# Optimization experiments

Measured on AMD Instinct MI355X. Metric: run time of the kernel, lower is better.

Reference implementation:

```python
import jax, jax.numpy as jnp
import numpy as np

N_NODES = 100000
DEG = 32
N_EDGES = N_NODES * DEG
N_FEAT = 128
N_CLASSES = 40
LN_EPS = 1e-5
CLAMP_MIN = 1e-5


def setup_inputs() -> dict:
    key = jax.random.key(0)
    k_h, k_lg, k_z, k_src, k_t1, k_t2 = jax.random.split(key, 6)
    h = jax.random.normal(k_h, (N_NODES, N_FEAT), dtype=jnp.float32)
    logits = jax.random.normal(k_lg, (N_NODES, N_CLASSES), dtype=jnp.float32)
    old_z = jax.random.uniform(k_z, (N_NODES,), dtype=jnp.float32)
    # uniform in-degree graph: every node receives exactly DEG messages
    dst = jnp.repeat(jnp.arange(N_NODES, dtype=jnp.int32), DEG)
    src = jax.random.randint(k_src, (N_EDGES,), 0, N_NODES, dtype=jnp.int32)
    in_degs = jnp.full((N_NODES,), float(DEG), dtype=jnp.float32)
    norm = 1.0 / in_degs  # GCN-style normalization constant per node
    tau_1 = jax.random.uniform(k_t1, (1,), dtype=jnp.float32)
    tau_2 = jax.random.uniform(k_t2, (1,), dtype=jnp.float32)
    return {"h": h, "logits": logits, "old_z": old_z, "norm": norm,
            "in_degs": in_degs, "tau_1": tau_1, "tau_2": tau_2,
            "src": src, "dst": dst}


def _node_layernorm(x):
    # LayerNorm over the node dimension, no affine (elementwise_affine=False)
    m = jnp.mean(x)
    v = jnp.var(x)
    return (x - m) * jax.lax.rsqrt(v + LN_EPS)


def reference(h, logits, old_z, norm, in_degs, tau_1, tau_2, src, dst):
    n = h.shape[0]
    c = logits.shape[1]
    # per-node predicted class, and per-edge neighbor prediction
    pred = jnp.argmax(logits, axis=1)            # [N]
    nbr_pred = pred[src]                          # [E]
    # f1: fraction of in-neighbors agreeing with the center node's prediction
    match = (nbr_pred == pred[dst]).astype(h.dtype)
    f1 = jax.ops.segment_sum(match, dst, num_segments=n) / in_degs
    # f2: entropy of the neighbor-prediction histogram per node
    counts = jnp.zeros((n, c), dtype=h.dtype).at[dst, nbr_pred].add(1.0)
    cnts_p = jnp.clip(counts / in_degs[:, None], CLAMP_MIN)
    f2 = -jnp.sum(cnts_p * jnp.log(cnts_p), axis=1)
    # both metrics are detached in the original
    f1 = jax.lax.stop_gradient(f1)
    f2 = jax.lax.stop_gradient(f2)
    norm_f1 = _node_layernorm(f1)
    norm_f2 = _node_layernorm(f2)
    # shared_tau=True path: uses externally provided tau_1 / tau_2
    z = jax.nn.sigmoid(-(norm_f1 - tau_1)) * jax.nn.sigmoid(-(norm_f2 - tau_2))
    gate = jnp.minimum(old_z, z)
    # sum aggregation of neighbor features, normalized and activated
    agg = jax.ops.segment_sum(h[src], dst, num_segments=n)   # [N, F]
    normagg = jax.nn.relu(agg * norm[:, None])
    new_h = h + gate[:, None] * normagg
    return new_h, z
```

## Files before the change

### kernel.cpp

```cpp
#include <hip/hip_runtime.h>
#include <math.h>

#define N_NODES 100000
#define DEG 32
#define N_FEAT 128
#define N_CLASSES 40

constexpr float LN_EPS = 1e-5f;
constexpr float E0 = 1.1512925465e-4f;

#define NODE_ITERS 8
#define NODES_PER_BLOCK 64
#define NB2 ((N_NODES + NODES_PER_BLOCK - 1) / NODES_PER_BLOCK)

#define NCHUNK 4
#define AGG_NPB 192
#define NBLK ((N_NODES + AGG_NPB - 1) / AGG_NPB)

typedef float    f4 __attribute__((ext_vector_type(4)));
typedef float    f2 __attribute__((ext_vector_type(2)));
typedef int      i4 __attribute__((ext_vector_type(4)));
typedef unsigned u2 __attribute__((ext_vector_type(2)));
typedef unsigned u4 __attribute__((ext_vector_type(4)));

__device__ __forceinline__ unsigned pk4_fp8(float a, float b, float c, float d) {
    int w = __builtin_amdgcn_cvt_pk_fp8_f32(a, b, 0, false);
    w = __builtin_amdgcn_cvt_pk_fp8_f32(c, d, w, true);
    return (unsigned)w;
}
__device__ __forceinline__ void accp8(float* a, u2 r) {
    f2 p;
    p = __builtin_amdgcn_cvt_pk_f32_fp8((int)r.x, false); a[0] += p.x; a[1] += p.y;
    p = __builtin_amdgcn_cvt_pk_f32_fp8((int)r.x, true);  a[2] += p.x; a[3] += p.y;
    p = __builtin_amdgcn_cvt_pk_f32_fp8((int)r.y, false); a[4] += p.x; a[5] += p.y;
    p = __builtin_amdgcn_cvt_pk_f32_fp8((int)r.y, true);  a[6] += p.x; a[7] += p.y;
}

__global__ void k_prep(const float* __restrict__ logits, const float* __restrict__ h,
                       const float* __restrict__ old_z, const float* __restrict__ normv,
                       unsigned char* __restrict__ predb, f2* __restrict__ ozn,
                       unsigned char* __restrict__ hb8, int do_pack) {
    int t = blockIdx.x * 256 + threadIdx.x;
    if (t >= N_NODES * 4) return;
    int node = t >> 2;
    int q    = t & 3;

    const f2* lp = (const f2*)(logits + (size_t)node * N_CLASSES + q * 10);
    float best = -INFINITY;
    int bidx = 0;
#pragma unroll
    for (int i = 0; i < 5; ++i) {
        f2 v = lp[i];
        int i0 = q * 10 + 2 * i;
        if (v.x > best) { best = v.x; bidx = i0; }
        if (v.y > best) { best = v.y; bidx = i0 + 1; }
    }
#pragma unroll
    for (int off = 1; off < 4; off <<= 1) {
        float ov = __shfl_xor(best, off, 4);
        int   oi = __shfl_xor(bidx, off, 4);
        if (ov > best || (ov == best && oi < bidx)) { best = ov; bidx = oi; }
    }
    if (q == 0) {
        predb[node] = (unsigned char)bidx;
        f2 oz; oz.x = old_z[node]; oz.y = normv[node];
        ozn[node] = oz;
    }

    if (do_pack) {
        const f4* hp = (const f4*)(h + (size_t)node * N_FEAT + q * 32);
        f4 v0 = __builtin_nontemporal_load(hp + 0);
        f4 v1 = __builtin_nontemporal_load(hp + 1);
        f4 v2 = __builtin_nontemporal_load(hp + 2);
        f4 v3 = __builtin_nontemporal_load(hp + 3);
        f4 v4 = __builtin_nontemporal_load(hp + 4);
        f4 v5 = __builtin_nontemporal_load(hp + 5);
        f4 v6 = __builtin_nontemporal_load(hp + 6);
        f4 v7 = __builtin_nontemporal_load(hp + 7);
        u4 o0, o1;
        o0.x = pk4_fp8(v0.x, v0.y, v0.z, v0.w);
        o0.y = pk4_fp8(v1.x, v1.y, v1.z, v1.w);
        o0.z = pk4_fp8(v2.x, v2.y, v2.z, v2.w);
        o0.w = pk4_fp8(v3.x, v3.y, v3.z, v3.w);
        o1.x = pk4_fp8(v4.x, v4.y, v4.z, v4.w);
        o1.y = pk4_fp8(v5.x, v5.y, v5.z, v5.w);
        o1.z = pk4_fp8(v6.x, v6.y, v6.z, v6.w);
        o1.w = pk4_fp8(v7.x, v7.y, v7.z, v7.w);
        u4* op = (u4*)(hb8 + ((size_t)q * N_NODES + node) * 32);
        op[0] = o0;
        op[1] = o1;
    }
}

__global__ void k_f1f2(const int* __restrict__ src,
                       const unsigned char* __restrict__ predb,
                       f2* __restrict__ f12, float* __restrict__ part) {
    const int tid  = threadIdx.x;
    const int lane = tid & 63;
    const int wave = tid >> 6;
    const int grp  = lane >> 5;
    const int j    = lane & 31;

    float acc_s1 = 0.f, acc_q1 = 0.f, acc_s2 = 0.f, acc_q2 = 0.f;

    for (int t = 0; t < NODE_ITERS; ++t) {
        int node = blockIdx.x * NODES_PER_BLOCK + t * 8 + wave * 2 + grp;
        if (node < N_NODES) {
            int s = src[node * DEG + j];
            int v = predb[s];
            int pv = predb[node];
            int c = 0;
#pragma unroll
            for (int k = 0; k < 32; ++k)
                c += (v == __shfl(v, k, 32)) ? 1 : 0;
            float cf = (float)c;
            float p  = cf * (1.0f / 32.0f);
            float ent  = (-p * logf(p)) / cf;
            float dstc = 1.0f / cf;
            float mt   = (v == pv) ? 1.0f : 0.0f;
#pragma unroll
            for (int off = 16; off >= 1; off >>= 1) {
                mt   += __shfl_xor(mt, off, 32);
                ent  += __shfl_xor(ent, off, 32);
                dstc += __shfl_xor(dstc, off, 32);
            }
            if (j == 0) {
                float f1v = mt * (1.0f / 32.0f);
                float f2v = ent + ((float)N_CLASSES - dstc) * E0;
                f2 o; o.x = f1v; o.y = f2v;
                f12[node] = o;
                acc_s1 += f1v; acc_q1 += f1v * f1v;
                acc_s2 += f2v; acc_q2 += f2v * f2v;
            }
        }
    }

#pragma unroll
    for (int off = 1; off < 64; off <<= 1) {
        acc_s1 += __shfl_xor(acc_s1, off);
        acc_q1 += __shfl_xor(acc_q1, off);
        acc_s2 += __shfl_xor(acc_s2, off);
        acc_q2 += __shfl_xor(acc_q2, off);
    }
    __shared__ float4 sred[4];
    if (lane == 0) sred[wave] = make_float4(acc_s1, acc_q1, acc_s2, acc_q2);
    __syncthreads();
    if (tid == 0) {
        float4 r = sred[0];
        for (int w = 1; w < 4; ++w) {
            float4 q = sred[w];
            r.x += q.x; r.y += q.y; r.z += q.z; r.w += q.w;
        }
        part[0 * NB2 + blockIdx.x] = r.x;
        part[1 * NB2 + blockIdx.x] = r.y;
        part[2 * NB2 + blockIdx.x] = r.z;
        part[3 * NB2 + blockIdx.x] = r.w;
    }
}

__global__ void k_scal(const float* __restrict__ part, float* __restrict__ scal,
                       int* __restrict__ ctr) {
    const int tid = threadIdx.x;
    if (tid < 16) ctr[tid] = 0;
    double s1 = 0, q1 = 0, s2 = 0, q2 = 0;
    for (int i = tid; i < NB2; i += 256) {
        s1 += (double)part[0 * NB2 + i];
        q1 += (double)part[1 * NB2 + i];
        s2 += (double)part[2 * NB2 + i];
        q2 += (double)part[3 * NB2 + i];
    }
    __shared__ double sd[256][4];
    sd[tid][0] = s1; sd[tid][1] = q1; sd[tid][2] = s2; sd[tid][3] = q2;
    __syncthreads();
    for (int st = 128; st > 0; st >>= 1) {
        if (tid < st) {
            sd[tid][0] += sd[tid + st][0];
            sd[tid][1] += sd[tid + st][1];
            sd[tid][2] += sd[tid + st][2];
            sd[tid][3] += sd[tid + st][3];
        }
        __syncthreads();
    }
    if (tid == 0) {
        double n = (double)N_NODES;
        double m1 = sd[0][0] / n, v1 = sd[0][1] / n - m1 * m1;
        double m2 = sd[0][2] / n, v2 = sd[0][3] / n - m2 * m2;
        scal[0] = (float)m1;
        scal[1] = (float)(1.0 / sqrt(v1 + (double)LN_EPS));
        scal[2] = (float)m2;
        scal[3] = (float)(1.0 / sqrt(v2 + (double)LN_EPS));
    }
}

__global__ __launch_bounds__(256, 2) void k_aggc(
        const unsigned char* __restrict__ hb8, const float* __restrict__ h,
        const int* __restrict__ src, const f2* __restrict__ f12,
        const f2* __restrict__ ozn, const float* __restrict__ scal,
        const float* __restrict__ tau1, const float* __restrict__ tau2,
        int* __restrict__ ctr, float* __restrict__ out_h,
        float* __restrict__ out_z) {
    __shared__ int s_item;
    if (threadIdx.x == 0) {
        unsigned xcd;
        asm volatile("s_getreg_b32 %0, hwreg(HW_REG_XCC_ID)" : "=s"(xcd));
        xcd &= 3;
        int item = -1;
        for (int a = 0; a < NCHUNK; ++a) {
            int cc = (int)((xcd + a) & 3);
            int t = atomicAdd(&ctr[cc], 1);
            if (t < NBLK) { item = (cc << 16) | t; break; }
        }
        s_item = item;
    }
    __syncthreads();
    int item = s_item;
    if (item < 0) return;
    const int chunk = item >> 16;
    const int nb    = item & 0xffff;
    const int g = threadIdx.x >> 2;
    const int j = threadIdx.x & 3;

    const int nodeA = nb * AGG_NPB + g;
    const int nodeB = nodeA + 64;
    const int nodeC = nodeA + 128;
    const bool hasC = (nodeC < N_NODES);
    const int nodeCc = hasC ? nodeC : nodeA;

    const i4* src4 = (const i4*)src;
    const u2* base = (const u2*)(hb8 + (size_t)chunk * ((size_t)N_NODES * 32));

    const float m1 = scal[0], i1 = scal[1], m2 = scal[2], i2 = scal[3];
    const float t1 = tau1[0], t2 = tau2[0];

    i4 svA0 = __builtin_nontemporal_load(&src4[nodeA * 8 + j * 2]);
    i4 svA1 = __builtin_nontemporal_load(&src4[nodeA * 8 + j * 2 + 1]);
    i4 svB0 = __builtin_nontemporal_load(&src4[nodeB * 8 + j * 2]);
    i4 svB1 = __builtin_nontemporal_load(&src4[nodeB * 8 + j * 2 + 1]);
    i4 svC0 = __builtin_nontemporal_load(&src4[nodeCc * 8 + j * 2]);
    i4 svC1 = __builtin_nontemporal_load(&src4[nodeCc * 8 + j * 2 + 1]);

    const f4* hpA = (const f4*)(h + (size_t)nodeA * N_FEAT + chunk * 32 + j * 8);
    f4 hA0 = __builtin_nontemporal_load(hpA);
    f4 hA1 = __builtin_nontemporal_load(hpA + 1);
    const f4* hpB = (const f4*)(h + (size_t)nodeB * N_FEAT + chunk * 32 + j * 8);
    f4 hB0 = __builtin_nontemporal_load(hpB);
    f4 hB1 = __builtin_nontemporal_load(hpB + 1);
    const f4* hpC = (const f4*)(h + (size_t)nodeCc * N_FEAT + chunk * 32 + j * 8);
    f4 hC0 = __builtin_nontemporal_load(hpC);
    f4 hC1 = __builtin_nontemporal_load(hpC + 1);
    f2 fvA = f12[nodeA], ozA = ozn[nodeA];
    f2 fvB = f12[nodeB], ozB = ozn[nodeB];
    f2 fvC = f12[nodeCc], ozC = ozn[nodeCc];

    float aA[8], aB[8], aC[8];
#pragma unroll
    for (int q = 0; q < 8; ++q) { aA[q] = 0.f; aB[q] = 0.f; aC[q] = 0.f; }

#pragma unroll
    for (int o = 0; o < 4; ++o) {
        int a0 = __shfl(svA0.x, o, 4), a1 = __shfl(svA0.y, o, 4);
        int a2 = __shfl(svA0.z, o, 4), a3 = __shfl(svA0.w, o, 4);
        int a4 = __shfl(svA1.x, o, 4), a5 = __shfl(svA1.y, o, 4);
        int a6 = __shfl(svA1.z, o, 4), a7 = __shfl(svA1.w, o, 4);
        u2 rA0 = base[(unsigned)(a0 * 4 + j)];
        u2 rA1 = base[(unsigned)(a1 * 4 + j)];
        u2 rA2 = base[(unsigned)(a2 * 4 + j)];
        u2 rA3 = base[(unsigned)(a3 * 4 + j)];
        u2 rA4 = base[(unsigned)(a4 * 4 + j)];
        u2 rA5 = base[(unsigned)(a5 * 4 + j)];
        u2 rA6 = base[(unsigned)(a6 * 4 + j)];
        u2 rA7 = base[(unsigned)(a7 * 4 + j)];
        int b0 = __shfl(svB0.x, o, 4), b1 = __shfl(svB0.y, o, 4);
        int b2 = __shfl(svB0.z, o, 4), b3 = __shfl(svB0.w, o, 4);
        int b4 = __shfl(svB1.x, o, 4), b5 = __shfl(svB1.y, o, 4);
        int b6 = __shfl(svB1.z, o, 4), b7 = __shfl(svB1.w, o, 4);
        u2 rB0 = base[(unsigned)(b0 * 4 + j)];
        u2 rB1 = base[(unsigned)(b1 * 4 + j)];
        u2 rB2 = base[(unsigned)(b2 * 4 + j)];
        u2 rB3 = base[(unsigned)(b3 * 4 + j)];
        u2 rB4 = base[(unsigned)(b4 * 4 + j)];
        u2 rB5 = base[(unsigned)(b5 * 4 + j)];
        u2 rB6 = base[(unsigned)(b6 * 4 + j)];
        u2 rB7 = base[(unsigned)(b7 * 4 + j)];
        int c0 = __shfl(svC0.x, o, 4), c1 = __shfl(svC0.y, o, 4);
        int c2 = __shfl(svC0.z, o, 4), c3 = __shfl(svC0.w, o, 4);
        int c4 = __shfl(svC1.x, o, 4), c5 = __shfl(svC1.y, o, 4);
        int c6 = __shfl(svC1.z, o, 4), c7 = __shfl(svC1.w, o, 4);
        u2 rC0 = base[(unsigned)(c0 * 4 + j)];
        u2 rC1 = base[(unsigned)(c1 * 4 + j)];
        u2 rC2 = base[(unsigned)(c2 * 4 + j)];
        u2 rC3 = base[(unsigned)(c3 * 4 + j)];
        u2 rC4 = base[(unsigned)(c4 * 4 + j)];
        u2 rC5 = base[(unsigned)(c5 * 4 + j)];
        u2 rC6 = base[(unsigned)(c6 * 4 + j)];
        u2 rC7 = base[(unsigned)(c7 * 4 + j)];
        accp8(aA, rA0); accp8(aA, rA1); accp8(aA, rA2); accp8(aA, rA3);
        accp8(aA, rA4); accp8(aA, rA5); accp8(aA, rA6); accp8(aA, rA7);
        accp8(aB, rB0); accp8(aB, rB1); accp8(aB, rB2); accp8(aB, rB3);
        accp8(aB, rB4); accp8(aB, rB5); accp8(aB, rB6); accp8(aB, rB7);
        accp8(aC, rC0); accp8(aC, rC1); accp8(aC, rC2); accp8(aC, rC3);
        accp8(aC, rC4); accp8(aC, rC5); accp8(aC, rC6); accp8(aC, rC7);
    }

#define EPILOG(NODE, FV, OZ, H0, H1, AV, DO_STORE) \
    if (DO_STORE) { \
        float nf1 = (FV.x - m1) * i1; \
        float nf2 = (FV.y - m2) * i2; \
        float z = (1.0f / (1.0f + expf(nf1 - t1))) * \
                  (1.0f / (1.0f + expf(nf2 - t2))); \
        float gg = fminf(OZ.x, z) * OZ.y; \
        f4 o0, o1; \
        o0.x = H0.x + gg * fmaxf(AV[0], 0.f); \
        o0.y = H0.y + gg * fmaxf(AV[1], 0.f); \
        o0.z = H0.z + gg * fmaxf(AV[2], 0.f); \
        o0.w = H0.w + gg * fmaxf(AV[3], 0.f); \
        o1.x = H1.x + gg * fmaxf(AV[4], 0.f); \
        o1.y = H1.y + gg * fmaxf(AV[5], 0.f); \
        o1.z = H1.z + gg * fmaxf(AV[6], 0.f); \
        o1.w = H1.w + gg * fmaxf(AV[7], 0.f); \
        f4* op = (f4*)(out_h + (size_t)(NODE) * N_FEAT + chunk * 32 + j * 8); \
        __builtin_nontemporal_store(o0, op); \
        __builtin_nontemporal_store(o1, op + 1); \
        if (chunk == 0 && j == 0) out_z[NODE] = z; \
    }

    EPILOG(nodeA, fvA, ozA, hA0, hA1, aA, true)
    EPILOG(nodeB, fvB, ozB, hB0, hB1, aB, true)
    EPILOG(nodeC, fvC, ozC, hC0, hC1, aC, hasC)
#undef EPILOG
}

__global__ void k_agg(const float* __restrict__ h, const f2* __restrict__ ozn,
                      const int* __restrict__ src, const f2* __restrict__ f12,
                      const float* __restrict__ scal, const float* __restrict__ tau1,
                      const float* __restrict__ tau2,
                      float* __restrict__ out_h, float* __restrict__ out_z) {
    const int lane = threadIdx.x & 63;
    const int wave = threadIdx.x >> 6;
    const int grp  = lane >> 5;
    const int j    = lane & 31;
    const int node = blockIdx.x * 8 + wave * 2 + grp;
    if (node >= N_NODES) return;

    int sv = src[node * DEG + j];
    const float4* H4 = reinterpret_cast<const float4*>(h);
    float4 acc = make_float4(0.f, 0.f, 0.f, 0.f);
#pragma unroll
    for (int k = 0; k < DEG; ++k) {
        int s = __shfl(sv, k, 32);
        float4 r = H4[(size_t)s * (N_FEAT / 4) + j];
        acc.x += r.x; acc.y += r.y; acc.z += r.z; acc.w += r.w;
    }
    f2 fv = f12[node];
    f2 oz = ozn[node];
    float nf1 = (fv.x - scal[0]) * scal[1];
    float nf2 = (fv.y - scal[2]) * scal[3];
    float z = (1.0f / (1.0f + expf(nf1 - tau1[0]))) *
              (1.0f / (1.0f + expf(nf2 - tau2[0])));
    float gg = fminf(oz.x, z) * oz.y;
    float4 hrow = H4[(size_t)node * (N_FEAT / 4) + j];
    float4 o;
    o.x = hrow.x + gg * fmaxf(acc.x, 0.0f);
    o.y = hrow.y + gg * fmaxf(acc.y, 0.0f);
    o.z = hrow.z + gg * fmaxf(acc.z, 0.0f);
    o.w = hrow.w + gg * fmaxf(acc.w, 0.0f);
    reinterpret_cast<float4*>(out_h)[(size_t)node * (N_FEAT / 4) + j] = o;
    if (j == 0) out_z[node] = z;
}

extern "C" void kernel_launch(void* const* d_in, const int* in_sizes, int n_in,
                              void* d_out, int out_size, void* d_ws, size_t ws_size,
                              hipStream_t stream) {
    const float* h      = (const float*)d_in[0];
    const float* logits = (const float*)d_in[1];
    const float* old_z  = (const float*)d_in[2];
    const float* normv  = (const float*)d_in[3];
    const float* tau1   = (const float*)d_in[5];
    const float* tau2   = (const float*)d_in[6];
    const int*   src    = (const int*)d_in[7];

    float* out_h = (float*)d_out;
    float* out_z = out_h + (size_t)N_NODES * N_FEAT;

    float* w    = (float*)d_ws;
    f2*    f12  = (f2*)w;
    f2*    ozn  = f12 + N_NODES;
    float* part = (float*)(ozn + N_NODES);
    float* scal = part + 4 * NB2;
    int*   ctr  = (int*)(scal + 4);
    unsigned char* predb = (unsigned char*)(ctr + 16);
    size_t off_bytes = ((char*)(predb + N_NODES) - (char*)d_ws);
    off_bytes = (off_bytes + 255) & ~(size_t)255;
    unsigned char* hb8 = (unsigned char*)d_ws + off_bytes;
    size_t need = off_bytes + (size_t)N_NODES * N_FEAT;
    bool use_fp8 = (ws_size >= need);

    k_prep<<<(N_NODES * 4 + 255) / 256, 256, 0, stream>>>(logits, h, old_z, normv,
                                                          predb, ozn, hb8,
                                                          use_fp8 ? 1 : 0);
    k_f1f2<<<NB2, 256, 0, stream>>>(src, predb, f12, part);
    k_scal<<<1, 256, 0, stream>>>(part, scal, ctr);
    if (use_fp8) {
        k_aggc<<<NCHUNK * NBLK, 256, 0, stream>>>(hb8, h, src, f12, ozn, scal,
                                                  tau1, tau2, ctr, out_h, out_z);
    } else {
        k_agg<<<(N_NODES + 7) / 8, 256, 0, stream>>>(h, ozn, src, f12, scal,
                                                     tau1, tau2, out_h, out_z);
    }
}
```

Measured before the change: 167.0 us.

## Fuse scalar reduction into f1f2 via last-block atomic, ballot-based histogram counts

Removes the separate single-block k_scal launch. The last k_f1f2 block to finish, detected with an atomic counter that k_prep resets, now does the final double-precision reduction. It also replaces the 32-step shuffle compare loop for neighbor-class counts with six ballots on the class bits plus a popcount, and computes the match count with a ballot. The argmax load is widened to float4 reads. Risks include correct ordering of the counter reset across kernels and the fence semantics of the last-block pattern.

Measured after the change: 190.6 us. +14.1%, slower.

```diff
diff --git a/kernel.cpp b/kernel.cpp
--- a/kernel.cpp
+++ b/kernel.cpp
@@ -39,21 +39,38 @@
 __global__ void k_prep(const float* __restrict__ logits, const float* __restrict__ h,
                        const float* __restrict__ old_z, const float* __restrict__ normv,
                        unsigned char* __restrict__ predb, f2* __restrict__ ozn,
-                       unsigned char* __restrict__ hb8, int do_pack) {
+                       unsigned char* __restrict__ hb8, int* __restrict__ ctr,
+                       int do_pack) {
+    if (blockIdx.x == 0 && threadIdx.x == 0) ctr[8] = 0;
     int t = blockIdx.x * 256 + threadIdx.x;
     if (t >= N_NODES * 4) return;
     int node = t >> 2;
     int q    = t & 3;
 
-    const f2* lp = (const f2*)(logits + (size_t)node * N_CLASSES + q * 10);
+    const f4* lp = (const f4*)(logits + (size_t)node * N_CLASSES);
     float best = -INFINITY;
     int bidx = 0;
-#pragma unroll
-    for (int i = 0; i < 5; ++i) {
-        f2 v = lp[i];
-        int i0 = q * 10 + 2 * i;
-        if (v.x > best) { best = v.x; bidx = i0; }
-        if (v.y > best) { best = v.y; bidx = i0 + 1; }
+    {
+        f4 va = lp[q];
+        int b0 = 4 * q;
+        if (va.x > best) { best = va.x; bidx = b0 + 0; }
+        if (va.y > best) { best = va.y; bidx = b0 + 1; }
+        if (va.z > best) { best = va.z; bidx = b0 + 2; }
+        if (va.w > best) { best = va.w; bidx = b0 + 3; }
+        f4 vb = lp[4 + q];
+        b0 = 16 + 4 * q;
+        if (vb.x > best) { best = vb.x; bidx = b0 + 0; }
+        if (vb.y > best) { best = vb.y; bidx = b0 + 1; }
+        if (vb.z > best) { best = vb.z; bidx = b0 + 2; }
+        if (vb.w > best) { best = vb.w; bidx = b0 + 3; }
+        if (q < 2) {
+            f4 vc = lp[8 + q];
+            b0 = 32 + 4 * q;
+            if (vc.x > best) { best = vc.x; bidx = b0 + 0; }
+            if (vc.y > best) { best = vc.y; bidx = b0 + 1; }
+            if (vc.z > best) { best = vc.z; bidx = b0 + 2; }
+            if (vc.w > best) { best = vc.w; bidx = b0 + 3; }
+        }
     }
 #pragma unroll
     for (int off = 1; off < 4; off <<= 1) {
@@ -94,12 +111,14 @@
 
 __global__ void k_f1f2(const int* __restrict__ src,
                        const unsigned char* __restrict__ predb,
-                       f2* __restrict__ f12, float* __restrict__ part) {
+                       f2* __restrict__ f12, float* __restrict__ part,
+                       float* __restrict__ scal, int* __restrict__ ctr) {
     const int tid  = threadIdx.x;
     const int lane = tid & 63;
     const int wave = tid >> 6;
     const int grp  = lane >> 5;
     const int j    = lane & 31;
+    const unsigned long long gmask = 0xFFFFFFFFull << (grp * 32);
 
     float acc_s1 = 0.f, acc_q1 = 0.f, acc_s2 = 0.f, acc_q2 = 0.f;
 
@@ -109,23 +128,25 @@
             int s = src[node * DEG + j];
             int v = predb[s];
             int pv = predb[node];
-            int c = 0;
-#pragma unroll
-            for (int k = 0; k < 32; ++k)
-                c += (v == __shfl(v, k, 32)) ? 1 : 0;
+            unsigned long long mm = ~0ull;
+#pragma unroll
+            for (int b = 0; b < 6; ++b) {
+                unsigned long long bb = __ballot((v >> b) & 1);
+                mm &= ((v >> b) & 1) ? bb : ~bb;
+            }
+            int c = __popcll(mm & gmask);
+            int mtc = __popcll(__ballot(v == pv) & gmask);
             float cf = (float)c;
             float p  = cf * (1.0f / 32.0f);
             float ent  = (-p * logf(p)) / cf;
             float dstc = 1.0f / cf;
-            float mt   = (v == pv) ? 1.0f : 0.0f;
 #pragma unroll
             for (int off = 16; off >= 1; off >>= 1) {
-                mt   += __shfl_xor(mt, off, 32);
                 ent  += __shfl_xor(ent, off, 32);
                 dstc += __shfl_xor(dstc, off, 32);
             }
             if (j == 0) {
-                float f1v = mt * (1.0f / 32.0f);
+                float f1v = (float)mtc * (1.0f / 32.0f);
                 float f2v = ent + ((float)N_CLASSES - dstc) * E0;
                 f2 o; o.x = f1v; o.y = f2v;
                 f12[node] = o;
@@ -143,6 +164,7 @@
         acc_q2 += __shfl_xor(acc_q2, off);
     }
     __shared__ float4 sred[4];
+    __shared__ int s_last;
     if (lane == 0) sred[wave] = make_float4(acc_s1, acc_q1, acc_s2, acc_q2);
     __syncthreads();
     if (tid == 0) {
@@ -155,13 +177,15 @@
         part[1 * NB2 + blockIdx.x] = r.y;
         part[2 * NB2 + blockIdx.x] = r.z;
         part[3 * NB2 + blockIdx.x] = r.w;
-    }
-}
-
-__global__ void k_scal(const float* __restrict__ part, float* __restrict__ scal,
-                       int* __restrict__ ctr) {
-    const int tid = threadIdx.x;
-    if (tid < 16) ctr[tid] = 0;
+        __threadfence();
+        int d = atomicAdd(&ctr[8], 1);
+        s_last = (d == NB2 - 1) ? 1 : 0;
+    }
+    __syncthreads();
+    if (!s_last) return;
+
+    __threadfence();
+    if (tid < 8) ctr[tid] = 0;
     double s1 = 0, q1 = 0, s2 = 0, q2 = 0;
     for (int i = tid; i < NB2; i += 256) {
         s1 += (double)part[0 * NB2 + i];
@@ -396,10 +420,9 @@
     bool use_fp8 = (ws_size >= need);
 
     k_prep<<<(N_NODES * 4 + 255) / 256, 256, 0, stream>>>(logits, h, old_z, normv,
-                                                          predb, ozn, hb8,
+                                                          predb, ozn, hb8, ctr,
                                                           use_fp8 ? 1 : 0);
-    k_f1f2<<<NB2, 256, 0, stream>>>(src, predb, f12, part);
-    k_scal<<<1, 256, 0, stream>>>(part, scal, ctr);
+    k_f1f2<<<NB2, 256, 0, stream>>>(src, predb, f12, part, scal, ctr);
     if (use_fp8) {
         k_aggc<<<NCHUNK * NBLK, 256, 0, stream>>>(hb8, h, src, f12, ozn, scal,
                                                   tau1, tau2, ctr, out_h, out_z);
```
